# Kernel tuning notes

Measured on AMD Instinct MI355X. Metric: run time of the kernel, lower is better.

## Reference

```python
import jax, jax.numpy as jnp
import numpy as np

D = 1024
NHEAD = 16
HEAD_DIM = D // NHEAD


def setup_inputs() -> dict:
    key = jax.random.key(0)
    ks = jax.random.split(key, 7)
    B, L = 4, 2048
    q = jax.random.normal(ks[0], (B, L, D), dtype=jnp.float32)
    k = jax.random.normal(ks[1], (B, L, D), dtype=jnp.float32)
    v = jax.random.normal(ks[2], (B, L, D), dtype=jnp.float32)
    # packed QKV projection, as in nn.MultiheadAttention (in_proj_weight: [3d, d])
    scale = 1.0 / np.sqrt(D)
    in_proj_w = jax.random.uniform(ks[3], (3 * D, D), dtype=jnp.float32, minval=-scale, maxval=scale)
    in_proj_b = jnp.zeros((3 * D,), dtype=jnp.float32)
    out_w = jax.random.uniform(ks[4], (D, D), dtype=jnp.float32, minval=-scale, maxval=scale)
    out_b = jnp.zeros((D,), dtype=jnp.float32)
    return {"q": q, "k": k, "v": v, "in_proj_w": in_proj_w, "in_proj_b": in_proj_b,
            "out_w": out_w, "out_b": out_b}


def reference(q, k, v, in_proj_w, in_proj_b, out_w, out_b):
    # FP32 MHA, need_weights=True (average over heads), eval mode (dropout inactive).
    B, Lq, d = q.shape
    Lk = k.shape[1]
    # packed in-projection: rows [0:d] -> Q, [d:2d] -> K, [2d:3d] -> V
    qp = q @ in_proj_w[:d].T + in_proj_b[:d]
    kp = k @ in_proj_w[d:2 * d].T + in_proj_b[d:2 * d]
    vp = v @ in_proj_w[2 * d:].T + in_proj_b[2 * d:]
    # split heads: [B, H, L, hd]
    qp = qp.reshape(B, Lq, NHEAD, HEAD_DIM).transpose(0, 2, 1, 3)
    kp = kp.reshape(B, Lk, NHEAD, HEAD_DIM).transpose(0, 2, 1, 3)
    vp = vp.reshape(B, Lk, NHEAD, HEAD_DIM).transpose(0, 2, 1, 3)
    scores = jnp.einsum('bhqd,bhkd->bhqk', qp, kp) / jnp.sqrt(jnp.float32(HEAD_DIM))
    attn = jax.nn.softmax(scores, axis=-1)          # [B, H, Lq, Lk]
    ctx = jnp.einsum('bhqk,bhkd->bhqd', attn, vp)    # [B, H, Lq, hd]
    ctx = ctx.transpose(0, 2, 1, 3).reshape(B, Lq, d)
    out = ctx @ out_w.T + out_b                      # [B, Lq, d]
    weights = attn.mean(axis=1)                      # average over heads -> [B, Lq, Lk]
    return out, weights
```

## Files before the change

kernel.cpp:

```cpp
#include <hip/hip_runtime.h>
#include <hip/hip_bf16.h>

#define D_ 1024
#define NH 16
#define HD 64
#define B_ 4
#define L_ 2048
#define N_ (B_*L_)
#define BH_ (B_*NH)
#define SCALE_ 0.125f

typedef __bf16 bf16_t;
typedef __bf16 bf16x4 __attribute__((ext_vector_type(4)));
typedef __bf16 bf16x8 __attribute__((ext_vector_type(8)));
typedef float f32x4 __attribute__((ext_vector_type(4)));

typedef const __attribute__((address_space(1))) char gas_t;
typedef __attribute__((address_space(3))) char las_t;

__device__ __forceinline__ f32x4 mfma_bf16(bf16x8 a, bf16x8 b, f32x4 c) {
    return __builtin_amdgcn_mfma_f32_16x16x32_bf16(a, b, c, 0, 0, 0);
}

__device__ __forceinline__ bf16x8 cvt8_f32(const float* __restrict__ p) {
    const float4* p4 = reinterpret_cast<const float4*>(p);
    float4 a = p4[0], b = p4[1];
    bf16x8 r;
    r[0] = (bf16_t)a.x; r[1] = (bf16_t)a.y; r[2] = (bf16_t)a.z; r[3] = (bf16_t)a.w;
    r[4] = (bf16_t)b.x; r[5] = (bf16_t)b.y; r[6] = (bf16_t)b.z; r[7] = (bf16_t)b.w;
    return r;
}

__device__ __forceinline__ bf16x8 ld8_bf16(const bf16_t* __restrict__ p) {
    return *reinterpret_cast<const bf16x8*>(p);
}

__global__ __launch_bounds__(256) void k_cvt(const float* __restrict__ src,
                                             bf16_t* __restrict__ dst, int n8) {
    int i = blockIdx.x * blockDim.x + threadIdx.x;
    int stride = gridDim.x * blockDim.x;
    for (; i < n8; i += stride)
        *reinterpret_cast<bf16x8*>(dst + (size_t)i * 8) = cvt8_f32(src + (size_t)i * 8);
}

template<int MODE>
__global__ __launch_bounds__(256) void k_gemm(
    const bf16_t* __restrict__ A, const bf16_t* __restrict__ Bm,
    const float* __restrict__ bias,
    bf16_t* __restrict__ dst_bf, float* __restrict__ dst_f32)
{
    __shared__ __align__(16) char lds[2][8192];
    int tid  = threadIdx.x;
    int lane = tid & 63, w = tid >> 6;
    int r = lane & 15, g = lane >> 4;
    int wr = w >> 1, wc = w & 1;

    int bid = blockIdx.x;
    int swz = (bid & 7) * 64 + (bid >> 3);
    int tm = swz >> 3, tn = swz & 7;

    const bf16_t* Ab = A  + (size_t)tm * 128 * 1024;
    const bf16_t* Bb = Bm + (size_t)tn * 128 * 1024;

    f32x4 z = {0.f, 0.f, 0.f, 0.f};
    f32x4 acc[4][4];
    #pragma unroll
    for (int m = 0; m < 4; ++m)
        #pragma unroll
        for (int n = 0; n < 4; ++n) acc[m][n] = z;

    for (int k0 = 0; k0 < 1024; k0 += 32) {
        #pragma unroll
        for (int i = 0; i < 2; ++i) {
            int o = i * 4096 + tid * 16;
            int row = o >> 6;
            int lchunk = ((o >> 4) & 3) ^ (row & 3);
            const bf16_t* gA = Ab + (size_t)row * 1024 + k0 + lchunk * 8;
            const bf16_t* gB = Bb + (size_t)row * 1024 + k0 + lchunk * 8;
            char* lpA = &lds[0][0] + i * 4096 + w * 1024;
            char* lpB = &lds[1][0] + i * 4096 + w * 1024;
            __builtin_amdgcn_global_load_lds((gas_t*)gA, (las_t*)lpA, 16, 0, 0);
            __builtin_amdgcn_global_load_lds((gas_t*)gB, (las_t*)lpB, 16, 0, 0);
        }
        __syncthreads();

        bf16x8 af[4], bf_[4];
        #pragma unroll
        for (int m = 0; m < 4; ++m) {
            int R = wr * 64 + m * 16 + r;
            af[m] = *reinterpret_cast<const bf16x8*>(
                &lds[0][0] + R * 64 + (((g ^ (R & 3)) << 4)));
        }
        #pragma unroll
        for (int n = 0; n < 4; ++n) {
            int R = wc * 64 + n * 16 + r;
            bf_[n] = *reinterpret_cast<const bf16x8*>(
                &lds[1][0] + R * 64 + (((g ^ (R & 3)) << 4)));
        }
        #pragma unroll
        for (int m = 0; m < 4; ++m)
            #pragma unroll
            for (int n = 0; n < 4; ++n)
                acc[m][n] = mfma_bf16(af[m], bf_[n], acc[m][n]);
        __syncthreads();
    }

    #pragma unroll
    for (int m = 0; m < 4; ++m)
        #pragma unroll
        for (int n = 0; n < 4; ++n)
            #pragma unroll
            for (int i = 0; i < 4; ++i) {
                int row = tm * 128 + wr * 64 + m * 16 + g * 4 + i;
                int col = tn * 128 + wc * 64 + n * 16 + r;
                float val = acc[m][n][i] + bias[col];
                if (MODE == 3) {
                    dst_f32[(size_t)row * 1024 + col] = val;
                } else {
                    int bb = row >> 11, ln = row & 2047;
                    int h = col >> 6, dd = col & 63;
                    if (MODE == 2)
                        dst_bf[(((size_t)(bb * NH + h)) * HD + dd) * L_ + ln] = (bf16_t)val;
                    else
                        dst_bf[(((size_t)(bb * NH + h)) * L_ + ln) * HD + dd] = (bf16_t)val;
                }
            }
}

__global__ __launch_bounds__(256, 2) void k_attn(
    const bf16_t* __restrict__ qp, const bf16_t* __restrict__ kp,
    const bf16_t* __restrict__ vpT,
    bf16_t* __restrict__ ctx, float* __restrict__ mOut, float* __restrict__ lInvOut)
{
    __shared__ __align__(16) char sK[2][8192];
    __shared__ __align__(16) char sV[2][8192];
    __shared__ __align__(16) char sP[4][4096];

    int tid  = threadIdx.x;
    int w    = tid >> 6;
    int lane = tid & 63;
    int r = lane & 15, g = lane >> 4;
    int bh = blockIdx.x & 63;
    int qg = blockIdx.x >> 6;
    int qbase = qg * 128 + w * 32;

    const bf16_t* qpb = qp  + (size_t)bh * L_ * HD;
    const bf16_t* kpb = kp  + (size_t)bh * L_ * HD;
    const bf16_t* vtb = vpT + (size_t)bh * HD * L_;

    bf16x8 bq[2][2];
    #pragma unroll
    for (int qt = 0; qt < 2; ++qt)
        #pragma unroll
        for (int ds = 0; ds < 2; ++ds)
            bq[qt][ds] = ld8_bf16(qpb + (size_t)(qbase + qt * 16 + r) * HD + ds * 32 + g * 8);

    f32x4 z = {0.f, 0.f, 0.f, 0.f};
    f32x4 acc[2][4];
    #pragma unroll
    for (int qt = 0; qt < 2; ++qt)
        #pragma unroll
        for (int dt = 0; dt < 4; ++dt) acc[qt][dt] = z;
    float m_[2] = {-1e30f, -1e30f};
    float l_[2] = {0.f, 0.f};

    char* Pw = &sP[w][0];

    auto stage = [&](int buf, int k0) {
        #pragma unroll
        for (int i = 0; i < 2; ++i) {
            int row = i * 32 + (tid >> 3);
            int lc  = (tid & 7) ^ (row & 7);
            const bf16_t* gK = kpb + (size_t)(k0 + row) * HD + lc * 8;
            const bf16_t* gV = vtb + (size_t)row * L_ + k0 + lc * 8;
            __builtin_amdgcn_global_load_lds((gas_t*)gK,
                (las_t*)(&sK[buf][0] + i * 4096 + tid * 16), 16, 0, 0);
            __builtin_amdgcn_global_load_lds((gas_t*)gV,
                (las_t*)(&sV[buf][0] + i * 4096 + tid * 16), 16, 0, 0);
        }
    };

    stage(0, 0);
    __syncthreads();
    int buf = 0;

    for (int kt = 0; kt < 32; ++kt) {
        if (kt + 1 < 32) stage(buf ^ 1, (kt + 1) * 64);

        const char* Kb = &sK[buf][0];
        const char* Vb = &sV[buf][0];

        f32x4 sT[4][2];
        #pragma unroll
        for (int ktile = 0; ktile < 4; ++ktile) {
            bf16x8 a0 = *reinterpret_cast<const bf16x8*>(
                Kb + (ktile * 16 + r) * 128 + (((g    ) ^ (r & 7)) << 4));
            bf16x8 a1 = *reinterpret_cast<const bf16x8*>(
                Kb + (ktile * 16 + r) * 128 + (((4 + g) ^ (r & 7)) << 4));
            #pragma unroll
            for (int qt = 0; qt < 2; ++qt) {
                f32x4 t = mfma_bf16(a0, bq[qt][0], z);
                sT[ktile][qt] = mfma_bf16(a1, bq[qt][1], t);
            }
        }

        float s[2][16], lm[2];
        #pragma unroll
        for (int qt = 0; qt < 2; ++qt) {
            #pragma unroll
            for (int ktile = 0; ktile < 4; ++ktile)
                #pragma unroll
                for (int i = 0; i < 4; ++i)
                    s[qt][ktile * 4 + i] = sT[ktile][qt][i] * SCALE_;
            float mx = s[qt][0];
            #pragma unroll
            for (int j = 1; j < 16; ++j) mx = fmaxf(mx, s[qt][j]);
            mx = fmaxf(mx, __shfl_xor(mx, 16));
            mx = fmaxf(mx, __shfl_xor(mx, 32));
            lm[qt] = mx;
        }
        bool need = (lm[0] > m_[0] + 8.f) || (lm[1] > m_[1] + 8.f);
        need = __any(need);
        if (need) {
            float alpha[2];
            #pragma unroll
            for (int qt = 0; qt < 2; ++qt) {
                float mn = fmaxf(m_[qt], lm[qt]);
                alpha[qt] = __expf(m_[qt] - mn);
                m_[qt] = mn;
                l_[qt] *= alpha[qt];
            }
            #pragma unroll
            for (int qt = 0; qt < 2; ++qt) {
                float av[4];
                #pragma unroll
                for (int i = 0; i < 4; ++i) av[i] = __shfl(alpha[qt], 4 * g + i);
                #pragma unroll
                for (int dt = 0; dt < 4; ++dt)
                    #pragma unroll
                    for (int i = 0; i < 4; ++i) acc[qt][dt][i] *= av[i];
            }
        }
        #pragma unroll
        for (int qt = 0; qt < 2; ++qt) {
            float ls = 0.f;
            #pragma unroll
            for (int ktile = 0; ktile < 4; ++ktile) {
                bf16x4 pw;
                #pragma unroll
                for (int i = 0; i < 4; ++i) {
                    float p = __expf(s[qt][ktile * 4 + i] - m_[qt]);
                    ls += p;
                    pw[i] = (bf16_t)p;
                }
                *reinterpret_cast<bf16x4*>(Pw + (qt * 16 + r) * 128 +
                    (((2 * ktile + (g >> 1)) ^ (r & 7)) << 4) + ((g & 1) << 3)) = pw;
            }
            ls += __shfl_xor(ls, 16);
            ls += __shfl_xor(ls, 32);
            l_[qt] += ls;
        }

        bf16x8 pa[2][2];
        #pragma unroll
        for (int qt = 0; qt < 2; ++qt)
            #pragma unroll
            for (int ks = 0; ks < 2; ++ks)
                pa[qt][ks] = *reinterpret_cast<const bf16x8*>(
                    Pw + (qt * 16 + r) * 128 + (((4 * ks + g) ^ (r & 7)) << 4));
        #pragma unroll
        for (int dt = 0; dt < 4; ++dt)
            #pragma unroll
            for (int ks = 0; ks < 2; ++ks) {
                bf16x8 bv = *reinterpret_cast<const bf16x8*>(
                    Vb + (dt * 16 + r) * 128 + (((4 * ks + g) ^ (r & 7)) << 4));
                acc[0][dt] = mfma_bf16(pa[0][ks], bv, acc[0][dt]);
                acc[1][dt] = mfma_bf16(pa[1][ks], bv, acc[1][dt]);
            }

        __syncthreads();
        buf ^= 1;
    }

    int bb = bh >> 4, h = bh & 15;
    #pragma unroll
    for (int qt = 0; qt < 2; ++qt) {
        float linv = 1.0f / l_[qt];
        float lq[4];
        #pragma unroll
        for (int i = 0; i < 4; ++i) lq[i] = __shfl(linv, 4 * g + i);
        #pragma unroll
        for (int i = 0; i < 4; ++i) {
            int q = qbase + qt * 16 + 4 * g + i;
            #pragma unroll
            for (int dt = 0; dt < 4; ++dt) {
                float val = acc[qt][dt][i] * lq[i];
                ctx[(((size_t)(bb * L_ + q)) * NH + h) * HD + dt * 16 + r] = (bf16_t)val;
            }
        }
        if (g == 0) {
            int q = qbase + qt * 16 + r;
            mOut[(size_t)bh * L_ + q]    = m_[qt];
            lInvOut[(size_t)bh * L_ + q] = 1.0f / l_[qt];
        }
    }
}

__global__ __launch_bounds__(256, 2) void k_weights(
    const bf16_t* __restrict__ qp, const bf16_t* __restrict__ kp,
    const float* __restrict__ mIn, const float* __restrict__ lInv,
    float* __restrict__ wout)
{
    __shared__ __align__(16) char sQ[2][16384];
    __shared__ __align__(16) char sKt[2][16384];
    __shared__ __align__(16) float sM[16][128];
    __shared__ __align__(16) float sLi[16][128];

    int tid  = threadIdx.x;
    int w    = tid >> 6;
    int lane = tid & 63;
    int r = lane & 15, g = lane >> 4;
    int wr = w >> 1, wc = w & 1;

    int wgid = (blockIdx.x & 7) * 128 + (blockIdx.x >> 3);
    int chunk = wgid >> 7;
    int b  = chunk >> 1;
    int qh = chunk & 1;
    int rem = wgid & 127;
    int qt = qh * 8 + (rem >> 4);
    int kt = rem & 15;
    int q0 = qt * 128, k0 = kt * 128;

    #pragma unroll
    for (int i = 0; i < 2; ++i) {
        int idx = i * 256 + tid;
        int h   = idx >> 5;
        int off = (idx & 31) * 4;
        const float* gm = mIn  + ((size_t)(b * NH + h) * L_ + q0 + off);
        const float* gl = lInv + ((size_t)(b * NH + h) * L_ + q0 + off);
        __builtin_amdgcn_global_load_lds((gas_t*)gm,
            (las_t*)((char*)&sM[0][0]  + i * 4096 + w * 1024), 16, 0, 0);
        __builtin_amdgcn_global_load_lds((gas_t*)gl,
            (las_t*)((char*)&sLi[0][0] + i * 4096 + w * 1024), 16, 0, 0);
    }

    auto stage_qk = [&](int buf, int h) {
        const bf16_t* Qh = qp + ((size_t)(b * NH + h) * L_ + q0) * HD;
        const bf16_t* Kh = kp + ((size_t)(b * NH + h) * L_ + k0) * HD;
        #pragma unroll
        for (int i = 0; i < 4; ++i) {
            int idx = i * 256 + tid;
            int row = idx >> 3;
            int lc  = (idx & 7) ^ (row & 7);
            const bf16_t* gQ = Qh + (size_t)row * HD + lc * 8;
            const bf16_t* gK = Kh + (size_t)row * HD + lc * 8;
            __builtin_amdgcn_global_load_lds((gas_t*)gQ,
                (las_t*)(&sQ[buf][0]  + i * 4096 + w * 1024), 16, 0, 0);
            __builtin_amdgcn_global_load_lds((gas_t*)gK,
                (las_t*)(&sKt[buf][0] + i * 4096 + w * 1024), 16, 0, 0);
        }
    };

    float acc[4][4][4] = {};
    f32x4 z = {0.f, 0.f, 0.f, 0.f};

    stage_qk(0, 0);
    __syncthreads();
    int buf = 0;

    for (int h = 0; h < NH; ++h) {
        if (h + 1 < NH) stage_qk(buf ^ 1, h + 1);

        const char* Qb = &sQ[buf][0];
        const char* Kb = &sKt[buf][0];

        bf16x8 bfrag[4][2];
        #pragma unroll
        for (int nf = 0; nf < 4; ++nf) {
            int R = wc * 64 + nf * 16 + r;
            bfrag[nf][0] = *reinterpret_cast<const bf16x8*>(
                Kb + R * 128 + (((g    ) ^ (R & 7)) << 4));
            bfrag[nf][1] = *reinterpret_cast<const bf16x8*>(
                Kb + R * 128 + (((4 + g) ^ (R & 7)) << 4));
        }
        #pragma unroll
        for (int mf = 0; mf < 4; ++mf) {
            int R = wr * 64 + mf * 16 + r;
            bf16x8 af0 = *reinterpret_cast<const bf16x8*>(
                Qb + R * 128 + (((g    ) ^ (R & 7)) << 4));
            bf16x8 af1 = *reinterpret_cast<const bf16x8*>(
                Qb + R * 128 + (((4 + g) ^ (R & 7)) << 4));
            int qrow = wr * 64 + mf * 16 + g * 4;
            f32x4 mv  = *reinterpret_cast<const f32x4*>(&sM[h][qrow]);
            f32x4 liv = *reinterpret_cast<const f32x4*>(&sLi[h][qrow]);
            #pragma unroll
            for (int nf = 0; nf < 4; ++nf) {
                f32x4 t = mfma_bf16(af0, bfrag[nf][0], z);
                t = mfma_bf16(af1, bfrag[nf][1], t);
                #pragma unroll
                for (int i = 0; i < 4; ++i)
                    acc[mf][nf][i] += __expf(t[i] * SCALE_ - mv[i]) * liv[i];
            }
        }
        __syncthreads();
        buf ^= 1;
    }

    const float inv_h = 1.0f / (float)NH;
    #pragma unroll
    for (int mf = 0; mf < 4; ++mf)
        #pragma unroll
        for (int nf = 0; nf < 4; ++nf)
            #pragma unroll
            for (int i = 0; i < 4; ++i) {
                int qidx = q0 + wr * 64 + mf * 16 + g * 4 + i;
                int kidx = k0 + wc * 64 + nf * 16 + r;
                wout[((size_t)(b * L_ + qidx)) * L_ + kidx] = acc[mf][nf][i] * inv_h;
            }
}

extern "C" void kernel_launch(void* const* d_in, const int* in_sizes, int n_in,
                              void* d_out, int out_size, void* d_ws, size_t ws_size,
                              hipStream_t stream) {
    const float* q     = (const float*)d_in[0];
    const float* k     = (const float*)d_in[1];
    const float* v     = (const float*)d_in[2];
    const float* in_w  = (const float*)d_in[3];
    const float* in_b  = (const float*)d_in[4];
    const float* out_w = (const float*)d_in[5];
    const float* out_b = (const float*)d_in[6];

    char* ws = (char*)d_ws;
    bf16_t* xb   = (bf16_t*)(ws);
    bf16_t* wb   = (bf16_t*)(ws + ((size_t)48 << 20));
    bf16_t* owb  = (bf16_t*)(ws + ((size_t)54 << 20));
    bf16_t* qp   = (bf16_t*)(ws + ((size_t)56 << 20));
    bf16_t* kp   = (bf16_t*)(ws + ((size_t)72 << 20));
    bf16_t* vpT  = (bf16_t*)(ws + ((size_t)88 << 20));
    bf16_t* ctx  = (bf16_t*)(ws + ((size_t)104 << 20));
    float*  mBuf = (float*)(ws + ((size_t)120 << 20));
    float*  lBuf = (float*)(ws + ((size_t)120 << 20) + (size_t)BH_ * L_ * 4);

    bf16_t* qb = xb;
    bf16_t* kb = xb + (size_t)N_ * D_;
    bf16_t* vb = xb + (size_t)2 * N_ * D_;

    float* outp = (float*)d_out;
    float* wout = outp + (size_t)N_ * D_;

    k_cvt<<<2048, 256, 0, stream>>>(q, qb, N_ * D_ / 8);
    k_cvt<<<2048, 256, 0, stream>>>(k, kb, N_ * D_ / 8);
    k_cvt<<<2048, 256, 0, stream>>>(v, vb, N_ * D_ / 8);
    k_cvt<<<1536, 256, 0, stream>>>(in_w, wb, 3 * D_ * D_ / 8);
    k_cvt<<<512,  256, 0, stream>>>(out_w, owb, D_ * D_ / 8);

    k_gemm<0><<<512, 256, 0, stream>>>(qb, wb,                   in_b,        qp,  nullptr);
    k_gemm<1><<<512, 256, 0, stream>>>(kb, wb + (size_t)D_*D_,   in_b + D_,   kp,  nullptr);
    k_gemm<2><<<512, 256, 0, stream>>>(vb, wb + (size_t)2*D_*D_, in_b + 2*D_, vpT, nullptr);

    k_attn   <<<1024, 256, 0, stream>>>(qp, kp, vpT, ctx, mBuf, lBuf);
    k_weights<<<1024, 256, 0, stream>>>(qp, kp, mBuf, lBuf, wout);

    k_gemm<3><<<512, 256, 0, stream>>>(ctx, owb, out_b, nullptr, outp);
}
```

Before: 325.0 us.

## Fold softmax scale and log2e into Q projection, sum probabilities via MFMA

Folds 1/sqrt(hd)*log2(e) into the Q projection epilogue so the attention and weights kernels can use raw exp2 without per-element scaling. The softmax row-sum is computed with an MFMA against a ones vector instead of per-lane adds and cross-lane shuffles. The five conversion launches are merged into two, and the K/V staging address arithmetic is hoisted out of the loop. This trades a bf16 rounding of the pre-scaled Q and a bf16-rounded P in the row sum for fewer VALU ops in the exp-heavy loops.

```diff
diff --git a/kernel.cpp b/kernel.cpp
--- a/kernel.cpp
+++ b/kernel.cpp
@@ -8,7 +8,8 @@
 #define L_ 2048
 #define N_ (B_*L_)
 #define BH_ (B_*NH)
-#define SCALE_ 0.125f
+#define QSCALE_ 0.18033688011112042f
+#define THR2_ 11.5f
 
 typedef __bf16 bf16_t;
 typedef __bf16 bf16x4 __attribute__((ext_vector_type(4)));
@@ -35,12 +36,38 @@
     return *reinterpret_cast<const bf16x8*>(p);
 }
 
-__global__ __launch_bounds__(256) void k_cvt(const float* __restrict__ src,
-                                             bf16_t* __restrict__ dst, int n8) {
+__global__ __launch_bounds__(256) void k_cvt3(
+    const float* __restrict__ s0, const float* __restrict__ s1,
+    const float* __restrict__ s2,
+    bf16_t* __restrict__ d0, bf16_t* __restrict__ d1, bf16_t* __restrict__ d2)
+{
+    const int n8 = N_ * D_ / 8;
     int i = blockIdx.x * blockDim.x + threadIdx.x;
     int stride = gridDim.x * blockDim.x;
-    for (; i < n8; i += stride)
-        *reinterpret_cast<bf16x8*>(dst + (size_t)i * 8) = cvt8_f32(src + (size_t)i * 8);
+    for (; i < 3 * n8; i += stride) {
+        int seg = i >> 20, off = i & (n8 - 1);
+        const float* s = (seg == 0) ? s0 : ((seg == 1) ? s1 : s2);
+        bf16_t* d      = (seg == 0) ? d0 : ((seg == 1) ? d1 : d2);
+        *reinterpret_cast<bf16x8*>(d + (size_t)off * 8) = cvt8_f32(s + (size_t)off * 8);
+    }
+}
+
+__global__ __launch_bounds__(256) void k_cvtw(
+    const float* __restrict__ w, const float* __restrict__ ow,
+    bf16_t* __restrict__ dw, bf16_t* __restrict__ dow)
+{
+    const int n8w = 3 * D_ * D_ / 8;
+    const int n8o = D_ * D_ / 8;
+    int i = blockIdx.x * blockDim.x + threadIdx.x;
+    int stride = gridDim.x * blockDim.x;
+    for (; i < n8w + n8o; i += stride) {
+        if (i < n8w)
+            *reinterpret_cast<bf16x8*>(dw + (size_t)i * 8) = cvt8_f32(w + (size_t)i * 8);
+        else {
+            int j = i - n8w;
+            *reinterpret_cast<bf16x8*>(dow + (size_t)j * 8) = cvt8_f32(ow + (size_t)j * 8);
+        }
+    }
 }
 
 template<int MODE>
@@ -114,6 +141,7 @@
                 int row = tm * 128 + wr * 64 + m * 16 + g * 4 + i;
                 int col = tn * 128 + wc * 64 + n * 16 + r;
                 float val = acc[m][n][i] + bias[col];
+                if (MODE == 0) val *= QSCALE_;
                 if (MODE == 3) {
                     dst_f32[(size_t)row * 1024 + col] = val;
                 } else {
@@ -155,27 +183,35 @@
         for (int ds = 0; ds < 2; ++ds)
             bq[qt][ds] = ld8_bf16(qpb + (size_t)(qbase + qt * 16 + r) * HD + ds * 32 + g * 8);
 
+    bf16x8 ones;
+    #pragma unroll
+    for (int i = 0; i < 8; ++i) ones[i] = (bf16_t)1.0f;
+
     f32x4 z = {0.f, 0.f, 0.f, 0.f};
     f32x4 acc[2][4];
     #pragma unroll
     for (int qt = 0; qt < 2; ++qt)
         #pragma unroll
         for (int dt = 0; dt < 4; ++dt) acc[qt][dt] = z;
+    f32x4 acc_l[2];
+    acc_l[0] = z; acc_l[1] = z;
     float m_[2] = {-1e30f, -1e30f};
-    float l_[2] = {0.f, 0.f};
 
     char* Pw = &sP[w][0];
 
+    int srow = tid >> 3;
+    int slc  = (tid & 7) ^ (srow & 7);
+    const bf16_t* gK0 = kpb + (size_t)srow * HD + slc * 8;
+    const bf16_t* gV0 = vtb + (size_t)srow * L_ + slc * 8;
+
     auto stage = [&](int buf, int k0) {
+        const bf16_t* gK = gK0 + (size_t)k0 * HD;
+        const bf16_t* gV = gV0 + k0;
         #pragma unroll
         for (int i = 0; i < 2; ++i) {
-            int row = i * 32 + (tid >> 3);
-            int lc  = (tid & 7) ^ (row & 7);
-            const bf16_t* gK = kpb + (size_t)(k0 + row) * HD + lc * 8;
-            const bf16_t* gV = vtb + (size_t)row * L_ + k0 + lc * 8;
-            __builtin_amdgcn_global_load_lds((gas_t*)gK,
+            __builtin_amdgcn_global_load_lds((gas_t*)(gK + (size_t)i * 32 * HD),
                 (las_t*)(&sK[buf][0] + i * 4096 + tid * 16), 16, 0, 0);
-            __builtin_amdgcn_global_load_lds((gas_t*)gV,
+            __builtin_amdgcn_global_load_lds((gas_t*)(gV + (size_t)i * 32 * L_),
                 (las_t*)(&sV[buf][0] + i * 4096 + tid * 16), 16, 0, 0);
         }
     };
@@ -204,61 +240,49 @@
             }
         }
 
-        float s[2][16], lm[2];
+        float lm[2];
         #pragma unroll
         for (int qt = 0; qt < 2; ++qt) {
+            float mx = sT[0][qt][0];
             #pragma unroll
             for (int ktile = 0; ktile < 4; ++ktile)
                 #pragma unroll
                 for (int i = 0; i < 4; ++i)
-                    s[qt][ktile * 4 + i] = sT[ktile][qt][i] * SCALE_;
-            float mx = s[qt][0];
-            #pragma unroll
-            for (int j = 1; j < 16; ++j) mx = fmaxf(mx, s[qt][j]);
+                    mx = fmaxf(mx, sT[ktile][qt][i]);
             mx = fmaxf(mx, __shfl_xor(mx, 16));
             mx = fmaxf(mx, __shfl_xor(mx, 32));
             lm[qt] = mx;
         }
-        bool need = (lm[0] > m_[0] + 8.f) || (lm[1] > m_[1] + 8.f);
+        bool need = (lm[0] > m_[0] + THR2_) || (lm[1] > m_[1] + THR2_);
         need = __any(need);
         if (need) {
-            float alpha[2];
             #pragma unroll
             for (int qt = 0; qt < 2; ++qt) {
                 float mn = fmaxf(m_[qt], lm[qt]);
-                alpha[qt] = __expf(m_[qt] - mn);
+                float alpha = __builtin_amdgcn_exp2f(m_[qt] - mn);
                 m_[qt] = mn;
-                l_[qt] *= alpha[qt];
-            }
-            #pragma unroll
-            for (int qt = 0; qt < 2; ++qt) {
                 float av[4];
                 #pragma unroll
-                for (int i = 0; i < 4; ++i) av[i] = __shfl(alpha[qt], 4 * g + i);
+                for (int i = 0; i < 4; ++i) av[i] = __shfl(alpha, 4 * g + i);
                 #pragma unroll
                 for (int dt = 0; dt < 4; ++dt)
                     #pragma unroll
                     for (int i = 0; i < 4; ++i) acc[qt][dt][i] *= av[i];
+                #pragma unroll
+                for (int i = 0; i < 4; ++i) acc_l[qt][i] *= av[i];
             }
         }
         #pragma unroll
         for (int qt = 0; qt < 2; ++qt) {
-            float ls = 0.f;
             #pragma unroll
             for (int ktile = 0; ktile < 4; ++ktile) {
                 bf16x4 pw;
                 #pragma unroll
-                for (int i = 0; i < 4; ++i) {
-                    float p = __expf(s[qt][ktile * 4 + i] - m_[qt]);
-                    ls += p;
-                    pw[i] = (bf16_t)p;
-                }
+                for (int i = 0; i < 4; ++i)
+                    pw[i] = (bf16_t)__builtin_amdgcn_exp2f(sT[ktile][qt][i] - m_[qt]);
                 *reinterpret_cast<bf16x4*>(Pw + (qt * 16 + r) * 128 +
                     (((2 * ktile + (g >> 1)) ^ (r & 7)) << 4) + ((g & 1) << 3)) = pw;
             }
-            ls += __shfl_xor(ls, 16);
-            ls += __shfl_xor(ls, 32);
-            l_[qt] += ls;
         }
 
         bf16x8 pa[2][2];
@@ -268,6 +292,11 @@
             for (int ks = 0; ks < 2; ++ks)
                 pa[qt][ks] = *reinterpret_cast<const bf16x8*>(
                     Pw + (qt * 16 + r) * 128 + (((4 * ks + g) ^ (r & 7)) << 4));
+        #pragma unroll
+        for (int qt = 0; qt < 2; ++qt) {
+            acc_l[qt] = mfma_bf16(pa[qt][0], ones, acc_l[qt]);
+            acc_l[qt] = mfma_bf16(pa[qt][1], ones, acc_l[qt]);
+        }
         #pragma unroll
         for (int dt = 0; dt < 4; ++dt)
             #pragma unroll
@@ -285,10 +314,9 @@
     int bb = bh >> 4, h = bh & 15;
     #pragma unroll
     for (int qt = 0; qt < 2; ++qt) {
-        float linv = 1.0f / l_[qt];
         float lq[4];
         #pragma unroll
-        for (int i = 0; i < 4; ++i) lq[i] = __shfl(linv, 4 * g + i);
+        for (int i = 0; i < 4; ++i) lq[i] = 1.0f / acc_l[qt][i];
         #pragma unroll
         for (int i = 0; i < 4; ++i) {
             int q = qbase + qt * 16 + 4 * g + i;
@@ -300,8 +328,14 @@
         }
         if (g == 0) {
             int q = qbase + qt * 16 + r;
-            mOut[(size_t)bh * L_ + q]    = m_[qt];
-            lInvOut[(size_t)bh * L_ + q] = 1.0f / l_[qt];
+            mOut[(size_t)bh * L_ + q] = m_[qt];
+        }
+        if (r == 0) {
+            #pragma unroll
+            for (int i = 0; i < 4; ++i) {
+                int q = qbase + qt * 16 + 4 * g + i;
+                lInvOut[(size_t)bh * L_ + q] = lq[i];
+            }
         }
     }
 }
@@ -399,7 +433,7 @@
                 t = mfma_bf16(af1, bfrag[nf][1], t);
                 #pragma unroll
                 for (int i = 0; i < 4; ++i)
-                    acc[mf][nf][i] += __expf(t[i] * SCALE_ - mv[i]) * liv[i];
+                    acc[mf][nf][i] += __builtin_amdgcn_exp2f(t[i] - mv[i]) * liv[i];
             }
         }
         __syncthreads();
@@ -448,11 +482,8 @@
     float* outp = (float*)d_out;
     float* wout = outp + (size_t)N_ * D_;
 
-    k_cvt<<<2048, 256, 0, stream>>>(q, qb, N_ * D_ / 8);
-    k_cvt<<<2048, 256, 0, stream>>>(k, kb, N_ * D_ / 8);
-    k_cvt<<<2048, 256, 0, stream>>>(v, vb, N_ * D_ / 8);
-    k_cvt<<<1536, 256, 0, stream>>>(in_w, wb, 3 * D_ * D_ / 8);
-    k_cvt<<<512,  256, 0, stream>>>(out_w, owb, D_ * D_ / 8);
+    k_cvt3<<<2048, 256, 0, stream>>>(q, k, v, qb, kb, vb);
+    k_cvtw<<<1024, 256, 0, stream>>>(in_w, out_w, wb, owb);
 
     k_gemm<0><<<512, 256, 0, stream>>>(qb, wb,                   in_b,        qp,  nullptr);
     k_gemm<1><<<512, 256, 0, stream>>>(kb, wb + (size_t)D_*D_,   in_b + D_,   kp,  nullptr);
```

Measured after the change: 306.1 us. 1.06x faster.
